# Kernel tuning notes

Measured on AMD Instinct MI355X. Metric: run time of the kernel, lower is better.

Reference implementation:

```python
import jax, jax.numpy as jnp
import numpy as np

N = 500_000      # total nodes (vehicles + obstacles)
NV = 400_000     # vehicles, stored as prefix rows [:NV]
E = 16_000_000   # directed edges

DT = 0.2
SAFE = 1.5
PARK = 5.0
RADIUS = 1.5
DEFV = 2.5
BOUND0 = 1.0
BOUND1 = 0.8
PI = np.pi


def setup_inputs() -> dict:
    key = jax.random.key(0)
    k1, k2, k3, k4, k5 = jax.random.split(key, 5)
    y_pred = jax.random.normal(k1, (NV, 2), jnp.float32)
    y_ref = jax.random.normal(k2, (NV, 2), jnp.float32)
    X = jax.random.normal(k3, (N, 9), jnp.float32)
    # type flag in last column: 0 = vehicle (prefix), 1 = obstacle
    type_col = jnp.concatenate([jnp.zeros(NV, jnp.float32), jnp.ones(N - NV, jnp.float32)])
    X_cur = X.at[:, 8].set(type_col)
    edges = jax.random.randint(k4, (2, E), 0, N, dtype=jnp.int32)
    be_static = jax.random.normal(k5, (NV, 2), jnp.float32)
    return {"y_pred": y_pred, "y_ref": y_ref, "X_cur": X_cur, "edges": edges, "be_static": be_static}


def _vehicle_dynamic(X, y, nv):
    # X: [N, 9], y: [nv, 2] controls (pedal, steer); vehicles are rows [:nv]
    cur = X[:nv]
    x_t = cur[:, 0] + cur[:, 3] * jnp.cos(cur[:, 2]) * DT
    y_t = cur[:, 1] + cur[:, 3] * jnp.sin(cur[:, 2]) * DT
    psi_t = cur[:, 2] + cur[:, 3] * DT * jnp.tan(y[:, 1]) / 2.0
    psi_t = (psi_t + PI) % (2 * PI) - PI
    v_t = 0.99 * cur[:, 3] + y[:, 0] * DT
    nxt = jnp.stack([x_t, y_t, psi_t, v_t], axis=-1)
    veh = jnp.concatenate([nxt, cur[:, 4:]], axis=1)
    return jnp.concatenate([veh, X[nv:]], axis=0)


def _loss_for_speed(X_ref, theta_ref, pedal_ref, pedal_pred, edges, nv, n):
    e0, e1 = edges[0], edges[1]
    veh_e = (e0 < nv).astype(X_ref.dtype)          # [E] edge-source-is-vehicle
    speed = X_ref[:, 3].at[:nv].add((pedal_pred - pedal_ref) * DT)  # [N]
    safe = jnp.abs(speed[e1]) + veh_e * jnp.abs(speed[e0]) + SAFE   # [E]
    vec = jnp.stack([jnp.cos(theta_ref), jnp.sin(theta_ref)], axis=-1)  # [nv,2]
    pos_pred_v = X_ref[:nv, :2] + vec * speed[:nv, None] * DT
    pos_pred = jnp.concatenate([pos_pred_v, X_ref[nv:, :2]], axis=0)    # [N,2]
    col7 = X_ref[:, 7]

    def col_loss(pos):
        d = jnp.linalg.norm(pos[e0] - pos[e1], axis=-1)
        lc = jax.nn.relu(safe + col7[e0] + (veh_e + 1.0) * RADIUS - d)
        lc = lc * lc + lc
        return jax.ops.segment_sum(lc, e1, num_segments=n)[:nv]

    loss_pred = jnp.linalg.norm(pos_pred_v, axis=-1) + col_loss(pos_pred)
    loss_ref = jnp.linalg.norm(X_ref[:nv, :2], axis=-1) + col_loss(X_ref[:, :2])
    d = loss_pred - loss_ref
    m = (d >= 0).astype(d.dtype)
    return (d * d + d) * m + d * (1.0 - m)


def reference(y_pred, y_ref, X_cur, edges, be_static):
    nv = y_pred.shape[0]
    n = X_cur.shape[0]
    X_ref = _vehicle_dynamic(X_cur, y_ref, nv)
    mask_1 = (jnp.linalg.norm(X_ref[:nv, :2] - X_cur[:nv, 4:6], axis=-1)
              - (PARK + jnp.abs(X_cur[:nv, 3]))) > 0
    mask_2 = jnp.abs(X_ref[:nv, 3]) >= DEFV - 1e-05
    mask_3 = jnp.sign(X_ref[:nv, 3]) * (y_ref[:, 0] - y_pred[:, 0]) <= 1e-05
    mask = (mask_1 & mask_2 & mask_3).astype(y_pred.dtype)

    loss_1 = jnp.mean(((y_ref[:, 1] - y_pred[:, 1]) / BOUND1) ** 2)
    loss_2_1 = ((y_ref[:, 0] - y_pred[:, 0]) / BOUND0) ** 2
    loss_2_2 = _loss_for_speed(X_ref, y_ref[:, 1], y_ref[:, 0], y_pred[:, 0], edges, nv, n)
    loss_2 = jnp.mean(loss_2_1 * (1.0 - mask) + loss_2_2 * mask)
    loss = loss_1 + loss_2

    bound = jnp.array([BOUND0, BOUND1], dtype=be_static.dtype)
    loss_3 = jnp.sum((be_static / bound) ** 2, axis=-1)
    loss = loss + jnp.mean(loss_3) * 0.1
    return loss
```

## Files before the change

kernel.cpp:

```cpp
#include <hip/hip_runtime.h>
#include <math.h>

#define NVEH 400000
#define NTOT 500000
#define NEDGE 16000000
#define DT 0.2f
#define SAFE_C 1.5f
#define PARK_C 5.0f
#define RADIUS_C 1.5f
#define DEFV_C 2.5f
#define LIST_CAP 4096
#define LIST_USE 128
#define REG_USE 16

#define NODE_BLOCKS ((NTOT + 255) / 256)
#define NODE_WAVES  (NODE_BLOCKS * 4)


__global__ __launch_bounds__(256) void node_kernel(
    const float* __restrict__ yp, const float* __restrict__ yr,
    const float* __restrict__ X, const float* __restrict__ be,
    float4* __restrict__ pos, float2* __restrict__ gh,
    float* __restrict__ basediff, float* __restrict__ maskArr,
    float* __restrict__ segdiff,
    int* __restrict__ countp, int* __restrict__ ids,
    double* __restrict__ partials)
{
    __shared__ float sX[256 * 9];
    int blk0 = blockIdx.x * 256;
    int nrows = NTOT - blk0; if (nrows > 256) nrows = 256;
    {
        int nf4 = (nrows * 9) >> 2;
        const float4* src = (const float4*)(X + (size_t)blk0 * 9);
        for (int t = threadIdx.x; t < nf4; t += 256)
            ((float4*)sX)[t] = src[t];
    }
    __syncthreads();

    int i = blk0 + threadIdx.x;
    double local = 0.0;
    if (i < NTOT) {
        const float* row = sX + threadIdx.x * 9;
        if (i < NVEH) {
            float x0 = row[0], x1 = row[1], psi = row[2], v = row[3];
            float p4 = row[4], p5 = row[5], x7 = row[7];
            float2 yrv = ((const float2*)yr)[i];
            float2 ypv = ((const float2*)yp)[i];
            float yr0 = yrv.x, yr1 = yrv.y, yp0 = ypv.x, yp1 = ypv.y;

            float xt = x0 + v * cosf(psi) * DT;
            float yt = x1 + v * sinf(psi) * DT;
            float vt = 0.99f * v + yr0 * DT;

            float speed = vt + (yp0 - yr0) * DT;
            float ct = cosf(yr1), st = sinf(yr1);
            float ppx = xt + ct * speed * DT;
            float ppy = yt + st * speed * DT;

            float as = fabsf(speed);
            pos[i] = make_float4(ppx, ppy, xt, yt);
            gh[i]  = make_float2(x7 + RADIUS_C + as + RADIUS_C, as + SAFE_C);

            float nrm_pred = sqrtf(ppx * ppx + ppy * ppy);
            float nrm_ref  = sqrtf(xt * xt + yt * yt);
            basediff[i] = nrm_pred - nrm_ref;

            float dx = xt - p4, dy = yt - p5;
            bool m1 = (sqrtf(dx * dx + dy * dy) - (PARK_C + fabsf(v))) > 0.0f;
            bool m2 = fabsf(vt) >= (DEFV_C - 1e-5f);
            float sg = (vt > 0.0f) ? 1.0f : ((vt < 0.0f) ? -1.0f : 0.0f);
            bool m3 = sg * (yr0 - yp0) <= 1e-5f;
            bool msk = m1 && m2 && m3;
            maskArr[i] = msk ? 1.0f : 0.0f;
            if (msk) {
                segdiff[i] = 0.0f;
                int idx = atomicAdd(countp, 1);
                if (idx < LIST_CAP) ids[idx] = i;
            }

            float t1 = (yr1 - yp1) * 1.25f;
            float l1 = t1 * t1;
            float t2 = yr0 - yp0;
            float l21 = t2 * t2;
            float2 bev = ((const float2*)be)[i];
            float b1s = bev.y * 1.25f;
            float l3 = bev.x * bev.x + b1s * b1s;

            local = (double)l1 + (double)((msk ? 0.0f : 1.0f) * l21) + 0.1 * (double)l3;
        } else {
            float x0 = row[0], x1 = row[1], v = row[3], x7 = row[7];
            pos[i] = make_float4(x0, x1, x0, x1);
            gh[i]  = make_float2(x7 + RADIUS_C, fabsf(v) + SAFE_C);
        }
    }
    for (int off = 32; off > 0; off >>= 1)
        local += __shfl_down(local, off, 64);
    if ((threadIdx.x & 63) == 0)
        partials[blockIdx.x * 4 + (threadIdx.x >> 6)] = local;
}

__device__ __forceinline__ void edge_compute(
    int a, int b, const float4* __restrict__ pos, const float2* __restrict__ gh,
    float* __restrict__ segdiff)
{
    float4 pa = pos[a];
    float4 pb = pos[b];
    float base = gh[a].x + gh[b].y;

    float dxp = pa.x - pb.x, dyp = pa.y - pb.y;
    float dp = sqrtf(dxp * dxp + dyp * dyp);
    float lcp = fmaxf(base - dp, 0.0f);

    float dxr = pa.z - pb.z, dyr = pa.w - pb.w;
    float dr = sqrtf(dxr * dxr + dyr * dyr);
    float lcr = fmaxf(base - dr, 0.0f);

    float diff = (lcp * lcp + lcp) - (lcr * lcr + lcr);
    if (diff != 0.0f)
        atomicAdd(segdiff + b, diff);
}

__global__ __launch_bounds__(256) void edge_kernel(
    const int* __restrict__ e0p, const int* __restrict__ e1p,
    const float4* __restrict__ pos, const float2* __restrict__ gh,
    const float* __restrict__ maskArr,
    float* __restrict__ segdiff,
    const int* __restrict__ countp, const int* __restrict__ ids)
{
    __shared__ int s_ids[LIST_USE];
    int cnt = *countp;
    int base = (blockIdx.x * 256 + threadIdx.x) * 4;

    if (cnt <= LIST_USE) {
        if (threadIdx.x < cnt) s_ids[threadIdx.x] = ids[threadIdx.x];
        __syncthreads();
        int4 bv = *(const int4*)(e1p + base);

        if (cnt <= REG_USE) {
            int idr[REG_USE];
#pragma unroll
            for (int j = 0; j < REG_USE; ++j)
                idr[j] = (j < cnt) ? s_ids[j] : -1;

            int bs[4] = {bv.x, bv.y, bv.z, bv.w};
#pragma unroll
            for (int k = 0; k < 4; ++k) {
                int b = bs[k];
                bool h = false;
#pragma unroll
                for (int j = 0; j < REG_USE; ++j) h |= (b == idr[j]);
                if (h) {
                    int a = e0p[base + k];
                    edge_compute(a, b, pos, gh, segdiff);
                }
            }
        } else {
            int bs[4] = {bv.x, bv.y, bv.z, bv.w};
#pragma unroll
            for (int k = 0; k < 4; ++k) {
                int b = bs[k];
                bool h = false;
                for (int j = 0; j < cnt; ++j) h |= (b == s_ids[j]);
                if (h) {
                    int a = e0p[base + k];
                    edge_compute(a, b, pos, gh, segdiff);
                }
            }
        }
    } else {
        for (int k = 0; k < 4; ++k) {
            int b = e1p[base + k];
            if (b < NVEH && maskArr[b] != 0.0f) {
                int a = e0p[base + k];
                edge_compute(a, b, pos, gh, segdiff);
            }
        }
    }
}

__global__ __launch_bounds__(256) void finish_kernel(
    const double* __restrict__ partials,
    const float* __restrict__ basediff, const float* __restrict__ segdiff,
    const float* __restrict__ maskArr,
    const int* __restrict__ countp, const int* __restrict__ ids,
    float* __restrict__ out)
{
    int tid = threadIdx.x;
    double s0 = 0.0, s1 = 0.0, s2 = 0.0, s3 = 0.0;
    for (int j = tid; j < NODE_WAVES; j += 1024) {
        s0 += partials[j];
        if (j + 256 < NODE_WAVES) s1 += partials[j + 256];
        if (j + 512 < NODE_WAVES) s2 += partials[j + 512];
        if (j + 768 < NODE_WAVES) s3 += partials[j + 768];
    }
    double s = (s0 + s1) + (s2 + s3);

    int cnt = *countp;
    if (cnt <= LIST_CAP) {
        for (int j = tid; j < cnt; j += 256) {
            int i = ids[j];
            float d = basediff[i] + segdiff[i];
            s += (double)((d >= 0.0f) ? (d * d + d) : d);
        }
    } else {
        for (int i = tid; i < NVEH; i += 256) {
            if (maskArr[i] != 0.0f) {
                float d = basediff[i] + segdiff[i];
                s += (double)((d >= 0.0f) ? (d * d + d) : d);
            }
        }
    }

    __shared__ double red[4];
    for (int off = 32; off > 0; off >>= 1)
        s += __shfl_down(s, off, 64);
    if ((tid & 63) == 0) red[tid >> 6] = s;
    __syncthreads();
    if (tid == 0) {
        double t = red[0] + red[1] + red[2] + red[3];
        out[0] = (float)(t * (1.0 / (double)NVEH));
    }
}

extern "C" void kernel_launch(void* const* d_in, const int* in_sizes, int n_in,
                              void* d_out, int out_size, void* d_ws, size_t ws_size,
                              hipStream_t stream) {
    const float* yp = (const float*)d_in[0];
    const float* yr = (const float*)d_in[1];
    const float* X  = (const float*)d_in[2];
    const int*   ed = (const int*)d_in[3];
    const float* be = (const float*)d_in[4];
    float* out = (float*)d_out;

    char* ws = (char*)d_ws;
    float4* pos      = (float4*)(ws + 0);
    float2* gh       = (float2*)(ws + 8000000);
    float*  basediff = (float*) (ws + 12000000);
    float*  maskArr  = (float*) (ws + 13600000);
    float*  segdiff  = (float*) (ws + 15200000);
    int*    countp   = (int*)   (ws + 16800000);
    int*    ids      = (int*)   (ws + 16800016);
    double* partials = (double*)(ws + 16816400);

    hipMemsetAsync(countp, 0, 4, stream);

    node_kernel<<<NODE_BLOCKS, 256, 0, stream>>>(
        yp, yr, X, be, pos, gh, basediff, maskArr, segdiff, countp, ids, partials);

    edge_kernel<<<NEDGE / (256 * 4), 256, 0, stream>>>(
        ed, ed + NEDGE, pos, gh, maskArr, segdiff, countp, ids);

    finish_kernel<<<1, 256, 0, stream>>>(
        partials, basediff, segdiff, maskArr, countp, ids, out);
}
```

Baseline: 203.2 us.

## Recompute node state on demand instead of materializing pos/gh arrays

The first kernel now covers only vehicle rows and computes just the mask and per-node loss terms. It no longer writes the pos/gh/basediff arrays for all 500k nodes. Edge and finish kernels recompute the needed node state from X, yr and yp for the few masked edges, which removes roughly 14 MB of writes. The shared-memory id list also grows to 4096 so the list path covers more masked counts, and e1 is read with nontemporal loads. The cost is extra trig work per processed edge and a larger serial loop over shared ids when the masked count is between 16 and 4096.

```diff
diff --git a/kernel.cpp b/kernel.cpp
--- a/kernel.cpp
+++ b/kernel.cpp
@@ -10,25 +10,52 @@
 #define RADIUS_C 1.5f
 #define DEFV_C 2.5f
 #define LIST_CAP 4096
-#define LIST_USE 128
 #define REG_USE 16
 
-#define NODE_BLOCKS ((NTOT + 255) / 256)
-#define NODE_WAVES  (NODE_BLOCKS * 4)
-
-
-__global__ __launch_bounds__(256) void node_kernel(
+#define MASK_BLOCKS ((NVEH + 255) / 256)
+#define MASK_WAVES  (MASK_BLOCKS * 4)
+
+typedef int vint4 __attribute__((ext_vector_type(4)));
+
+
+__device__ __forceinline__ void node_state(
+    int n, const float* __restrict__ X,
+    const float* __restrict__ yr, const float* __restrict__ yp,
+    float& px, float& py, float& rx, float& ry, float& g, float& h)
+{
+    const float* row = X + (size_t)n * 9;
+    float x0 = row[0], x1 = row[1], x7 = row[7];
+    if (n < NVEH) {
+        float psi = row[2], v = row[3];
+        float yr0 = yr[2 * n], yr1 = yr[2 * n + 1], yp0 = yp[2 * n];
+        float xt = x0 + v * cosf(psi) * DT;
+        float yt = x1 + v * sinf(psi) * DT;
+        float vt = 0.99f * v + yr0 * DT;
+        float speed = vt + (yp0 - yr0) * DT;
+        float as = fabsf(speed);
+        px = xt + cosf(yr1) * speed * DT;
+        py = yt + sinf(yr1) * speed * DT;
+        rx = xt; ry = yt;
+        g = x7 + RADIUS_C + as + RADIUS_C;
+        h = as + SAFE_C;
+    } else {
+        float v = row[3];
+        px = rx = x0; py = ry = x1;
+        g = x7 + RADIUS_C;
+        h = fabsf(v) + SAFE_C;
+    }
+}
+
+__global__ __launch_bounds__(256) void mask_kernel(
     const float* __restrict__ yp, const float* __restrict__ yr,
     const float* __restrict__ X, const float* __restrict__ be,
-    float4* __restrict__ pos, float2* __restrict__ gh,
-    float* __restrict__ basediff, float* __restrict__ maskArr,
-    float* __restrict__ segdiff,
+    float* __restrict__ maskArr, float* __restrict__ segdiff,
     int* __restrict__ countp, int* __restrict__ ids,
     double* __restrict__ partials)
 {
     __shared__ float sX[256 * 9];
     int blk0 = blockIdx.x * 256;
-    int nrows = NTOT - blk0; if (nrows > 256) nrows = 256;
+    int nrows = NVEH - blk0; if (nrows > 256) nrows = 256;
     {
         int nf4 = (nrows * 9) >> 2;
         const float4* src = (const float4*)(X + (size_t)blk0 * 9);
@@ -39,59 +66,40 @@
 
     int i = blk0 + threadIdx.x;
     double local = 0.0;
-    if (i < NTOT) {
+    if (i < NVEH) {
         const float* row = sX + threadIdx.x * 9;
-        if (i < NVEH) {
-            float x0 = row[0], x1 = row[1], psi = row[2], v = row[3];
-            float p4 = row[4], p5 = row[5], x7 = row[7];
-            float2 yrv = ((const float2*)yr)[i];
-            float2 ypv = ((const float2*)yp)[i];
-            float yr0 = yrv.x, yr1 = yrv.y, yp0 = ypv.x, yp1 = ypv.y;
-
-            float xt = x0 + v * cosf(psi) * DT;
-            float yt = x1 + v * sinf(psi) * DT;
-            float vt = 0.99f * v + yr0 * DT;
-
-            float speed = vt + (yp0 - yr0) * DT;
-            float ct = cosf(yr1), st = sinf(yr1);
-            float ppx = xt + ct * speed * DT;
-            float ppy = yt + st * speed * DT;
-
-            float as = fabsf(speed);
-            pos[i] = make_float4(ppx, ppy, xt, yt);
-            gh[i]  = make_float2(x7 + RADIUS_C + as + RADIUS_C, as + SAFE_C);
-
-            float nrm_pred = sqrtf(ppx * ppx + ppy * ppy);
-            float nrm_ref  = sqrtf(xt * xt + yt * yt);
-            basediff[i] = nrm_pred - nrm_ref;
-
-            float dx = xt - p4, dy = yt - p5;
-            bool m1 = (sqrtf(dx * dx + dy * dy) - (PARK_C + fabsf(v))) > 0.0f;
-            bool m2 = fabsf(vt) >= (DEFV_C - 1e-5f);
-            float sg = (vt > 0.0f) ? 1.0f : ((vt < 0.0f) ? -1.0f : 0.0f);
-            bool m3 = sg * (yr0 - yp0) <= 1e-5f;
-            bool msk = m1 && m2 && m3;
-            maskArr[i] = msk ? 1.0f : 0.0f;
-            if (msk) {
-                segdiff[i] = 0.0f;
-                int idx = atomicAdd(countp, 1);
-                if (idx < LIST_CAP) ids[idx] = i;
-            }
-
-            float t1 = (yr1 - yp1) * 1.25f;
-            float l1 = t1 * t1;
-            float t2 = yr0 - yp0;
-            float l21 = t2 * t2;
-            float2 bev = ((const float2*)be)[i];
-            float b1s = bev.y * 1.25f;
-            float l3 = bev.x * bev.x + b1s * b1s;
-
-            local = (double)l1 + (double)((msk ? 0.0f : 1.0f) * l21) + 0.1 * (double)l3;
-        } else {
-            float x0 = row[0], x1 = row[1], v = row[3], x7 = row[7];
-            pos[i] = make_float4(x0, x1, x0, x1);
-            gh[i]  = make_float2(x7 + RADIUS_C, fabsf(v) + SAFE_C);
-        }
+        float x0 = row[0], x1 = row[1], psi = row[2], v = row[3];
+        float p4 = row[4], p5 = row[5];
+        float2 yrv = ((const float2*)yr)[i];
+        float2 ypv = ((const float2*)yp)[i];
+        float yr0 = yrv.x, yr1 = yrv.y, yp0 = ypv.x, yp1 = ypv.y;
+
+        float xt = x0 + v * cosf(psi) * DT;
+        float yt = x1 + v * sinf(psi) * DT;
+        float vt = 0.99f * v + yr0 * DT;
+
+        float dx = xt - p4, dy = yt - p5;
+        bool m1 = (sqrtf(dx * dx + dy * dy) - (PARK_C + fabsf(v))) > 0.0f;
+        bool m2 = fabsf(vt) >= (DEFV_C - 1e-5f);
+        float sg = (vt > 0.0f) ? 1.0f : ((vt < 0.0f) ? -1.0f : 0.0f);
+        bool m3 = sg * (yr0 - yp0) <= 1e-5f;
+        bool msk = m1 && m2 && m3;
+        maskArr[i] = msk ? 1.0f : 0.0f;
+        if (msk) {
+            segdiff[i] = 0.0f;
+            int idx = atomicAdd(countp, 1);
+            if (idx < LIST_CAP) ids[idx] = i;
+        }
+
+        float t1 = (yr1 - yp1) * 1.25f;
+        float l1 = t1 * t1;
+        float t2 = yr0 - yp0;
+        float l21 = t2 * t2;
+        float2 bev = ((const float2*)be)[i];
+        float b1s = bev.y * 1.25f;
+        float l3 = bev.x * bev.x + b1s * b1s;
+
+        local = (double)l1 + (double)((msk ? 0.0f : 1.0f) * l21) + 0.1 * (double)l3;
     }
     for (int off = 32; off > 0; off >>= 1)
         local += __shfl_down(local, off, 64);
@@ -100,18 +108,22 @@
 }
 
 __device__ __forceinline__ void edge_compute(
-    int a, int b, const float4* __restrict__ pos, const float2* __restrict__ gh,
-    float* __restrict__ segdiff)
-{
-    float4 pa = pos[a];
-    float4 pb = pos[b];
-    float base = gh[a].x + gh[b].y;
-
-    float dxp = pa.x - pb.x, dyp = pa.y - pb.y;
+    int a, int b,
+    const float* __restrict__ X, const float* __restrict__ yr,
+    const float* __restrict__ yp, float* __restrict__ segdiff)
+{
+    float pax, pay, rax, ray, ga, ha;
+    float pbx, pby, rbx, rby, gb, hb;
+    node_state(a, X, yr, yp, pax, pay, rax, ray, ga, ha);
+    node_state(b, X, yr, yp, pbx, pby, rbx, rby, gb, hb);
+
+    float base = ga + hb;
+
+    float dxp = pax - pbx, dyp = pay - pby;
     float dp = sqrtf(dxp * dxp + dyp * dyp);
     float lcp = fmaxf(base - dp, 0.0f);
 
-    float dxr = pa.z - pb.z, dyr = pa.w - pb.w;
+    float dxr = rax - rbx, dyr = ray - rby;
     float dr = sqrtf(dxr * dxr + dyr * dyr);
     float lcr = fmaxf(base - dr, 0.0f);
 
@@ -122,19 +134,20 @@
 
 __global__ __launch_bounds__(256) void edge_kernel(
     const int* __restrict__ e0p, const int* __restrict__ e1p,
-    const float4* __restrict__ pos, const float2* __restrict__ gh,
-    const float* __restrict__ maskArr,
+    const float* __restrict__ X, const float* __restrict__ yr,
+    const float* __restrict__ yp, const float* __restrict__ maskArr,
     float* __restrict__ segdiff,
     const int* __restrict__ countp, const int* __restrict__ ids)
 {
-    __shared__ int s_ids[LIST_USE];
+    __shared__ int s_ids[LIST_CAP];
     int cnt = *countp;
     int base = (blockIdx.x * 256 + threadIdx.x) * 4;
 
-    if (cnt <= LIST_USE) {
-        if (threadIdx.x < cnt) s_ids[threadIdx.x] = ids[threadIdx.x];
+    if (cnt <= LIST_CAP) {
+        int lim = (cnt < LIST_CAP) ? cnt : LIST_CAP;
+        for (int t = threadIdx.x; t < lim; t += 256) s_ids[t] = ids[t];
         __syncthreads();
-        int4 bv = *(const int4*)(e1p + base);
+        vint4 bv = __builtin_nontemporal_load((const vint4*)(e1p + base));
 
         if (cnt <= REG_USE) {
             int idr[REG_USE];
@@ -151,7 +164,7 @@
                 for (int j = 0; j < REG_USE; ++j) h |= (b == idr[j]);
                 if (h) {
                     int a = e0p[base + k];
-                    edge_compute(a, b, pos, gh, segdiff);
+                    edge_compute(a, b, X, yr, yp, segdiff);
                 }
             }
         } else {
@@ -163,7 +176,7 @@
                 for (int j = 0; j < cnt; ++j) h |= (b == s_ids[j]);
                 if (h) {
                     int a = e0p[base + k];
-                    edge_compute(a, b, pos, gh, segdiff);
+                    edge_compute(a, b, X, yr, yp, segdiff);
                 }
             }
         }
@@ -172,7 +185,7 @@
             int b = e1p[base + k];
             if (b < NVEH && maskArr[b] != 0.0f) {
                 int a = e0p[base + k];
-                edge_compute(a, b, pos, gh, segdiff);
+                edge_compute(a, b, X, yr, yp, segdiff);
             }
         }
     }
@@ -180,18 +193,19 @@
 
 __global__ __launch_bounds__(256) void finish_kernel(
     const double* __restrict__ partials,
-    const float* __restrict__ basediff, const float* __restrict__ segdiff,
-    const float* __restrict__ maskArr,
+    const float* __restrict__ X, const float* __restrict__ yr,
+    const float* __restrict__ yp,
+    const float* __restrict__ segdiff, const float* __restrict__ maskArr,
     const int* __restrict__ countp, const int* __restrict__ ids,
     float* __restrict__ out)
 {
     int tid = threadIdx.x;
     double s0 = 0.0, s1 = 0.0, s2 = 0.0, s3 = 0.0;
-    for (int j = tid; j < NODE_WAVES; j += 1024) {
+    for (int j = tid; j < MASK_WAVES; j += 1024) {
         s0 += partials[j];
-        if (j + 256 < NODE_WAVES) s1 += partials[j + 256];
-        if (j + 512 < NODE_WAVES) s2 += partials[j + 512];
-        if (j + 768 < NODE_WAVES) s3 += partials[j + 768];
+        if (j + 256 < MASK_WAVES) s1 += partials[j + 256];
+        if (j + 512 < MASK_WAVES) s2 += partials[j + 512];
+        if (j + 768 < MASK_WAVES) s3 += partials[j + 768];
     }
     double s = (s0 + s1) + (s2 + s3);
 
@@ -199,13 +213,19 @@
     if (cnt <= LIST_CAP) {
         for (int j = tid; j < cnt; j += 256) {
             int i = ids[j];
-            float d = basediff[i] + segdiff[i];
+            float px, py, rx, ry, g, h;
+            node_state(i, X, yr, yp, px, py, rx, ry, g, h);
+            float bd = sqrtf(px * px + py * py) - sqrtf(rx * rx + ry * ry);
+            float d = bd + segdiff[i];
             s += (double)((d >= 0.0f) ? (d * d + d) : d);
         }
     } else {
         for (int i = tid; i < NVEH; i += 256) {
             if (maskArr[i] != 0.0f) {
-                float d = basediff[i] + segdiff[i];
+                float px, py, rx, ry, g, h;
+                node_state(i, X, yr, yp, px, py, rx, ry, g, h);
+                float bd = sqrtf(px * px + py * py) - sqrtf(rx * rx + ry * ry);
+                float d = bd + segdiff[i];
                 s += (double)((d >= 0.0f) ? (d * d + d) : d);
             }
         }
@@ -233,23 +253,20 @@
     float* out = (float*)d_out;
 
     char* ws = (char*)d_ws;
-    float4* pos      = (float4*)(ws + 0);
-    float2* gh       = (float2*)(ws + 8000000);
-    float*  basediff = (float*) (ws + 12000000);
-    float*  maskArr  = (float*) (ws + 13600000);
-    float*  segdiff  = (float*) (ws + 15200000);
-    int*    countp   = (int*)   (ws + 16800000);
-    int*    ids      = (int*)   (ws + 16800016);
-    double* partials = (double*)(ws + 16816400);
-
-    hipMemsetAsync(countp, 0, 4, stream);
-
-    node_kernel<<<NODE_BLOCKS, 256, 0, stream>>>(
-        yp, yr, X, be, pos, gh, basediff, maskArr, segdiff, countp, ids, partials);
+    float*  maskArr  = (float*) (ws + 0);
+    float*  segdiff  = (float*) (ws + 1600000);
+    int*    countp   = (int*)   (ws + 3200000);
+    int*    ids      = (int*)   (ws + 3200016);
+    double* partials = (double*)(ws + 3216400);
+
+    (void)hipMemsetAsync(countp, 0, 4, stream);
+
+    mask_kernel<<<MASK_BLOCKS, 256, 0, stream>>>(
+        yp, yr, X, be, maskArr, segdiff, countp, ids, partials);
 
     edge_kernel<<<NEDGE / (256 * 4), 256, 0, stream>>>(
-        ed, ed + NEDGE, pos, gh, maskArr, segdiff, countp, ids);
+        ed, ed + NEDGE, X, yr, yp, maskArr, segdiff, countp, ids);
 
     finish_kernel<<<1, 256, 0, stream>>>(
-        partials, basediff, segdiff, maskArr, countp, ids, out);
-}
+        partials, X, yr, yp, segdiff, maskArr, countp, ids, out);
+}
```

Measured after the change: 200.6 us. About the same (-1.3%).
